# Kernel tuning notes

Measured on AMD Instinct MI355X. Metric: run time of the kernel, lower is better.

The kernel has to match this reference:

```python
import jax, jax.numpy as jnp
import numpy as np

DIM = 1024
NUM_HEADS = 16
HEAD_DIM = DIM // NUM_HEADS
SCALE = HEAD_DIM ** (-0.5)


def setup_inputs() -> dict:
    key = jax.random.key(0)
    ks = jax.random.split(key, 5)
    B, N, C = 2, 2048, DIM
    q = jax.random.normal(ks[0], (B, N, C), dtype=jnp.float32)
    k = jax.random.normal(ks[1], (B, N, C), dtype=jnp.float32)
    v = jax.random.normal(ks[2], (B, N, C), dtype=jnp.float32)
    # fused qkv Linear weight, torch layout [3*C, C]; no bias (qkv_bias=False)
    qkv_w = jax.random.normal(ks[3], (3 * C, C), dtype=jnp.float32) * (C ** -0.5)
    proj_w = jax.random.normal(ks[4], (C, C), dtype=jnp.float32) * (C ** -0.5)
    proj_b = jnp.zeros((C,), dtype=jnp.float32)
    return {"q": q, "k": k, "v": v, "qkv_w": qkv_w, "proj_w": proj_w,
            "proj_b": proj_b, "use_mask": 1}


def reference(q, k, v, qkv_w, proj_w, proj_b, use_mask):
    B, N, C = q.shape
    N_k = k.shape[1]
    H, hd = NUM_HEADS, HEAD_DIM
    # The original applies the full fused qkv Linear to each of q,k,v and keeps
    # only slice 0/1/2 respectively; computing just the used slice is identical math.
    wq, wk, wv = qkv_w[:C], qkv_w[C:2 * C], qkv_w[2 * C:]
    qh = (q @ wq.T).reshape(B, N, H, hd).transpose(0, 2, 1, 3)      # [B,H,N,hd]
    kh = (k @ wk.T).reshape(B, N_k, H, hd).transpose(0, 2, 1, 3)    # [B,H,Nk,hd]
    vh = (v @ wv.T).reshape(B, N_k, H, hd).transpose(0, 2, 1, 3)    # [B,H,Nk,hd]
    attn = jnp.einsum('bhnd,bhmd->bhnm', qh, kh) * SCALE            # [B,H,N,Nk]
    if use_mask:  # static Python flag -> causal tril mask as in the source
        msk = jnp.tril(jnp.ones((N, N_k), dtype=bool))
        attn = jnp.where(msk[None, None], attn, jnp.float32(-1e9))
    attn = jax.nn.softmax(attn, axis=-1)
    x = jnp.einsum('bhnm,bhmd->bhnd', attn, vh)                     # [B,H,N,hd]
    x = x.transpose(0, 2, 1, 3).reshape(B, N, C)
    x = x @ proj_w.T + proj_b
    return x, attn
```

## Files before the change

### kernel.cpp

```cpp
#include <hip/hip_runtime.h>


typedef unsigned short u16;
typedef unsigned int u32;
typedef __attribute__((ext_vector_type(8))) short s16x8;
typedef __attribute__((ext_vector_type(4))) float f32x4;
typedef __attribute__((ext_vector_type(4))) u16 u16x4;

#define AS1 __attribute__((address_space(1)))
#define AS3 __attribute__((address_space(3)))

static __device__ __forceinline__ u16 f2bf(float f) {
  u32 u = __builtin_bit_cast(u32, f);
  u = (u + 0x7fffu + ((u >> 16) & 1u)) >> 16;
  return (u16)u;
}

static __device__ __forceinline__ void gll16(const u16* g, u16* l) {
  __builtin_amdgcn_global_load_lds((const AS1 u32*)g, (AS3 u32*)l, 16, 0, 0);
}

static __device__ __forceinline__ f32x4 mfma_bf16(s16x8 a, s16x8 b, f32x4 c) {
  return __builtin_amdgcn_mfma_f32_16x16x32_bf16(a, b, c, 0, 0, 0);
}

__global__ __launch_bounds__(256) void cast_all_kernel(
    const float* __restrict__ q, const float* __restrict__ k, const float* __restrict__ v,
    const float* __restrict__ qkv_w, const float* __restrict__ proj_w,
    u16* __restrict__ qb, u16* __restrict__ kb, u16* __restrict__ vb,
    u16* __restrict__ wb, u16* __restrict__ pwb) {
  int i = blockIdx.x * 256 + threadIdx.x;
  const float* src; u16* dst; int off;
  if (i < 1048576)       { src = q;      dst = qb;  off = i; }
  else if (i < 2097152)  { src = k;      dst = kb;  off = i - 1048576; }
  else if (i < 3145728)  { src = v;      dst = vb;  off = i - 2097152; }
  else if (i < 3932160)  { src = qkv_w;  dst = wb;  off = i - 3145728; }
  else if (i < 4194304)  { src = proj_w; dst = pwb; off = i - 3932160; }
  else return;
  f32x4 vv = ((const f32x4*)src)[off];
  u16x4 o = { f2bf(vv.x), f2bf(vv.y), f2bf(vv.z), f2bf(vv.w) };
  ((u16x4*)dst)[off] = o;
}

static __device__ __forceinline__ void gemm_core_1024(
    const u16* __restrict__ A, const u16* __restrict__ Bm,
    int m0, int n0, int t, u16* a_s, u16* b_s, f32x4 acc[4][4]) {
  const int lane = t & 63;
  const int w = t >> 6;
  const int wm = (w & 1) * 64, wn = (w >> 1) * 64;
  const int lrow = lane & 15, lq = lane >> 4;
  const int r0 = t >> 2;
  const int c0 = (t & 3) * 8;

  for (int kt = 0; kt < 1024; kt += 32) {
    __syncthreads();
    gll16(A  + (size_t)(m0 + r0)      * 1024 + kt + c0, &a_s[(size_t)t * 8]);
    gll16(A  + (size_t)(m0 + r0 + 64) * 1024 + kt + c0, &a_s[(size_t)(t + 256) * 8]);
    gll16(Bm + (size_t)(n0 + r0)      * 1024 + kt + c0, &b_s[(size_t)t * 8]);
    gll16(Bm + (size_t)(n0 + r0 + 64) * 1024 + kt + c0, &b_s[(size_t)(t + 256) * 8]);
    __syncthreads();
    s16x8 af[4], bfr[4];
#pragma unroll
    for (int x = 0; x < 4; x++) af[x]  = *(const s16x8*)&a_s[(wm + x*16 + lrow)*32 + lq*8];
#pragma unroll
    for (int x = 0; x < 4; x++) bfr[x] = *(const s16x8*)&b_s[(wn + x*16 + lrow)*32 + lq*8];
#pragma unroll
    for (int tm = 0; tm < 4; tm++)
#pragma unroll
      for (int tn = 0; tn < 4; tn++)
        acc[tm][tn] = mfma_bf16(af[tm], bfr[tn], acc[tm][tn]);
  }
}

__global__ __launch_bounds__(256) void gemm_qkv_kernel(
    const u16* __restrict__ qb, const u16* __restrict__ kb, const u16* __restrict__ vb,
    const u16* __restrict__ wb, u16* __restrict__ Qh, u16* __restrict__ Kh,
    u16* __restrict__ Vt) {
  __shared__ u16 a_s[128*32], b_s[128*32];
  const int mode = blockIdx.z;
  const u16* A = (mode == 0) ? qb : (mode == 1) ? kb : vb;
  const u16* Bm = wb + (size_t)mode * (1024 * 1024);
  const int m0 = blockIdx.y * 128, n0 = blockIdx.x * 128;
  const int t = threadIdx.x;
  f32x4 acc[4][4];
  const f32x4 Z = {0.f, 0.f, 0.f, 0.f};
#pragma unroll
  for (int i = 0; i < 4; i++)
#pragma unroll
    for (int j = 0; j < 4; j++) acc[i][j] = Z;

  gemm_core_1024(A, Bm, m0, n0, t, a_s, b_s, acc);

  const int lane = t & 63, w = t >> 6;
  const int wm = (w & 1) * 64, wn = (w >> 1) * 64;
  const int lrow = lane & 15, lq = lane >> 4;
#pragma unroll
  for (int tm = 0; tm < 4; tm++) {
#pragma unroll
    for (int tn = 0; tn < 4; tn++) {
      const int ng = n0 + wn + tn * 16 + lrow;
      const int h = ng >> 6, d = ng & 63;
#pragma unroll
      for (int i = 0; i < 4; i++) {
        const int mg = m0 + wm + tm * 16 + lq * 4 + i;
        const int b = mg >> 11, s = mg & 2047;
        const float v = acc[tm][tn][i];
        if (mode == 0)
          Qh[((size_t)(b * 16 + h) * 2048 + s) * 64 + d] = f2bf(v * 0.125f);
        else if (mode == 1)
          Kh[((size_t)(b * 16 + h) * 2048 + s) * 64 + d] = f2bf(v);
        else
          Vt[((size_t)(b * 16 + h) * 64 + d) * 2048 + s] = f2bf(v);
      }
    }
  }
}

__global__ __launch_bounds__(256) void gemm_proj_kernel(
    const u16* __restrict__ xatt, const u16* __restrict__ pwb,
    const float* __restrict__ bias, float* __restrict__ out) {
  __shared__ u16 a_s[128*32], b_s[128*32];
  const int m0 = blockIdx.y * 128, n0 = blockIdx.x * 128;
  const int t = threadIdx.x;
  f32x4 acc[4][4];
  const f32x4 Z = {0.f, 0.f, 0.f, 0.f};
#pragma unroll
  for (int i = 0; i < 4; i++)
#pragma unroll
    for (int j = 0; j < 4; j++) acc[i][j] = Z;

  gemm_core_1024(xatt, pwb, m0, n0, t, a_s, b_s, acc);

  const int lane = t & 63, w = t >> 6;
  const int wm = (w & 1) * 64, wn = (w >> 1) * 64;
  const int lrow = lane & 15, lq = lane >> 4;
#pragma unroll
  for (int tn = 0; tn < 4; tn++) {
    const int ng = n0 + wn + tn * 16 + lrow;
    const float bv = bias[ng];
#pragma unroll
    for (int tm = 0; tm < 4; tm++) {
#pragma unroll
      for (int i = 0; i < 4; i++) {
        const int mg = m0 + wm + tm * 16 + lq * 4 + i;
        out[(size_t)mg * 1024 + ng] = acc[tm][tn][i] + bv;
      }
    }
  }
}


static __device__ __forceinline__ void qk_tile(const s16x8 qf[2], const s16x8 kf[4][2],
                                               f32x4 sacc[4]) {
  const f32x4 Z = {0.f, 0.f, 0.f, 0.f};
#pragma unroll
  for (int tn = 0; tn < 4; tn++) {
    sacc[tn] = Z;
#pragma unroll
    for (int kq = 0; kq < 2; kq++)
      sacc[tn] = mfma_bf16(qf[kq], kf[tn][kq], sacc[tn]);
  }
}

static __device__ __forceinline__ void expsum_tile(const f32x4 sacc[4], bool diag,
                                                   int lrow, int rbase, float l_acc[4]) {
  float part[4] = {0.f, 0.f, 0.f, 0.f};
#pragma unroll
  for (int tn = 0; tn < 4; tn++)
#pragma unroll
    for (int i = 0; i < 4; i++) {
      const bool ok = !diag || (tn * 16 + lrow <= rbase + i);
      part[i] += ok ? __expf(sacc[tn][i]) : 0.f;
    }
#pragma unroll
  for (int i = 0; i < 4; i++) {
    float s = part[i];
    s += __shfl_xor(s, 1, 16);
    s += __shfl_xor(s, 2, 16);
    s += __shfl_xor(s, 4, 16);
    s += __shfl_xor(s, 8, 16);
    l_acc[i] += s;
  }
}

static __device__ __forceinline__ void p_phase(const f32x4 sacc[4], bool diag,
                                               int lane, int lrow, int lq, int w,
                                               const float invl[4], float* pw,
                                               float* __restrict__ gb, s16x8 pf[2]) {
#pragma unroll
  for (int tn = 0; tn < 4; tn++)
#pragma unroll
    for (int i = 0; i < 4; i++) {
      const int rl = lq * 4 + i;
      const bool ok = !diag || (tn * 16 + lrow <= w * 16 + rl);
      const float pv = ok ? __expf(sacc[tn][i]) * invl[i] : 0.f;
      pw[rl * 68 + tn * 16 + lrow] = pv;
    }
  const int rr = lane >> 3, c8 = (lane & 7) * 4;
#pragma unroll
  for (int j = 0; j < 2; j++)
#pragma unroll
    for (int m = 0; m < 2; m++) {
      f32x4 vv = *(const f32x4*)&pw[(rr + 8 * j) * 68 + m * 32 + c8];
      *(f32x4*)&gb[(size_t)(rr + 8 * j) * 2048 + m * 32 + c8] = vv;
    }
#pragma unroll
  for (int kq = 0; kq < 2; kq++) {
    f32x4 lo = *(const f32x4*)&pw[lrow * 68 + kq * 32 + lq * 8];
    f32x4 hi = *(const f32x4*)&pw[lrow * 68 + kq * 32 + lq * 8 + 4];
    s16x8 r;
    r[0] = (short)f2bf(lo.x); r[1] = (short)f2bf(lo.y);
    r[2] = (short)f2bf(lo.z); r[3] = (short)f2bf(lo.w);
    r[4] = (short)f2bf(hi.x); r[5] = (short)f2bf(hi.y);
    r[6] = (short)f2bf(hi.z); r[7] = (short)f2bf(hi.w);
    pf[kq] = r;
  }
}

__global__ __launch_bounds__(256, 2) void attn_kernel(
    const u16* __restrict__ Qh, const u16* __restrict__ Kh, const u16* __restrict__ Vt,
    float* __restrict__ attn, u16* __restrict__ xatt, const int* __restrict__ use_mask_p) {
  __shared__ u16 smem[8192 + 8192];
  __shared__ float p32[4][16 * 68];
  u16* k_s = smem;
  u16* vq  = smem + 8192;

  const int bh = blockIdx.y;
  const int p  = blockIdx.x;
  const int t = threadIdx.x;
  const int lane = t & 63, w = t >> 6;
  const int lrow = lane & 15, lq = lane >> 4;
  const int use_mask = *use_mask_p;

  const int q0[2] = { p * 64, (31 - p) * 64 };
  const int Tc[2] = { use_mask ? p : 31, use_mask ? 31 - p : 31 };
  const int Tmax  = Tc[1];

  const int rs  = t >> 3;
  const int csw = (((t & 7) ^ (rs & 7)) * 8);
  const int sk  = (lrow & 7) << 3;

  const u16* kg = Kh + (size_t)bh * (2048 * 64);
  const u16* vg = Vt + (size_t)bh * (64 * 2048);

  {
    const u16* qgA = Qh + ((size_t)bh * 2048 + q0[0]) * 64;
    const u16* qgB = Qh + ((size_t)bh * 2048 + q0[1]) * 64;
    gll16(qgA + (size_t)rs * 64 + csw,        &vq[t * 8]);
    gll16(qgA + (size_t)(rs + 32) * 64 + csw, &vq[(t + 256) * 8]);
    gll16(qgB + (size_t)rs * 64 + csw,        &vq[4096 + t * 8]);
    gll16(qgB + (size_t)(rs + 32) * 64 + csw, &vq[4096 + (t + 256) * 8]);
    gll16(kg + (size_t)rs * 64 + csw,         &k_s[t * 8]);
    gll16(kg + (size_t)(rs + 32) * 64 + csw,  &k_s[(t + 256) * 8]);
  }
  __syncthreads();

  s16x8 qf[2][2];
  const int qrow = w * 16 + lrow;
#pragma unroll
  for (int kq = 0; kq < 2; kq++) {
    qf[0][kq] = *(const s16x8*)&vq[qrow * 64 + ((kq * 32 + lq * 8) ^ sk)];
    qf[1][kq] = *(const s16x8*)&vq[4096 + qrow * 64 + ((kq * 32 + lq * 8) ^ sk)];
  }

  const int rbase = w * 16 + lq * 4;

  float l_acc[2][4];
#pragma unroll
  for (int c = 0; c < 2; c++)
#pragma unroll
    for (int i = 0; i < 4; i++) l_acc[c][i] = 0.f;

  for (int tt = 0; tt <= Tmax; tt++) {
    const int cur = tt & 1;
    if (tt < Tmax) {
      gll16(kg + (size_t)((tt + 1) * 64 + rs) * 64 + csw,      &k_s[(cur ^ 1) * 4096 + t * 8]);
      gll16(kg + (size_t)((tt + 1) * 64 + rs + 32) * 64 + csw, &k_s[(cur ^ 1) * 4096 + (t + 256) * 8]);
    }
    s16x8 kf[4][2];
#pragma unroll
    for (int tn = 0; tn < 4; tn++)
#pragma unroll
      for (int kq = 0; kq < 2; kq++)
        kf[tn][kq] = *(const s16x8*)&k_s[cur * 4096 + (tn * 16 + lrow) * 64 + ((kq * 32 + lq * 8) ^ sk)];
    f32x4 sacc[4];
    __builtin_amdgcn_s_setprio(1);
    qk_tile(qf[1], kf, sacc);
    __builtin_amdgcn_s_setprio(0);
    expsum_tile(sacc, use_mask && (tt == Tc[1]), lrow, rbase, l_acc[1]);
    if (tt <= Tc[0]) {
      __builtin_amdgcn_s_setprio(1);
      qk_tile(qf[0], kf, sacc);
      __builtin_amdgcn_s_setprio(0);
      expsum_tile(sacc, use_mask && (tt == Tc[0]), lrow, rbase, l_acc[0]);
    }
    __syncthreads();
  }

  float inv_l[2][4];
#pragma unroll
  for (int c = 0; c < 2; c++)
#pragma unroll
    for (int i = 0; i < 4; i++) inv_l[c][i] = 1.0f / l_acc[c][i];

  f32x4 oacc[2][4];
  const f32x4 Z = {0.f, 0.f, 0.f, 0.f};
#pragma unroll
  for (int c = 0; c < 2; c++)
#pragma unroll
    for (int i = 0; i < 4; i++) oacc[c][i] = Z;

  gll16(kg + (size_t)rs * 64 + csw,          &k_s[t * 8]);
  gll16(kg + (size_t)(rs + 32) * 64 + csw,   &k_s[(t + 256) * 8]);
  gll16(vg + (size_t)rs * 2048 + csw,        &vq[t * 8]);
  gll16(vg + (size_t)(rs + 32) * 2048 + csw, &vq[(t + 256) * 8]);
  __syncthreads();

  float* pw = &p32[w][0];

  for (int tt = 0; tt <= Tmax; tt++) {
    const int cur = tt & 1;
    if (tt < Tmax) {
      gll16(kg + (size_t)((tt + 1) * 64 + rs) * 64 + csw,        &k_s[(cur ^ 1) * 4096 + t * 8]);
      gll16(kg + (size_t)((tt + 1) * 64 + rs + 32) * 64 + csw,   &k_s[(cur ^ 1) * 4096 + (t + 256) * 8]);
      gll16(vg + (size_t)rs * 2048 + (tt + 1) * 64 + csw,        &vq[(cur ^ 1) * 4096 + t * 8]);
      gll16(vg + (size_t)(rs + 32) * 2048 + (tt + 1) * 64 + csw, &vq[(cur ^ 1) * 4096 + (t + 256) * 8]);
    }
    const bool act0 = (tt <= Tc[0]);
    s16x8 kf[4][2];
#pragma unroll
    for (int tn = 0; tn < 4; tn++)
#pragma unroll
      for (int kq = 0; kq < 2; kq++)
        kf[tn][kq] = *(const s16x8*)&k_s[cur * 4096 + (tn * 16 + lrow) * 64 + ((kq * 32 + lq * 8) ^ sk)];
    s16x8 vf[4][2];
#pragma unroll
    for (int td = 0; td < 4; td++)
#pragma unroll
      for (int kq = 0; kq < 2; kq++)
        vf[td][kq] = *(const s16x8*)&vq[cur * 4096 + (td * 16 + lrow) * 64 + ((kq * 32 + lq * 8) ^ sk)];

    {
      f32x4 sacc[4];
      __builtin_amdgcn_s_setprio(1);
      qk_tile(qf[1], kf, sacc);
      __builtin_amdgcn_s_setprio(0);
      s16x8 pf[2];
      float* gb = attn + ((size_t)(bh * 2048 + q0[1] + w * 16)) * 2048 + tt * 64;
      p_phase(sacc, use_mask && (tt == Tc[1]), lane, lrow, lq, w, inv_l[1], pw, gb, pf);
      __builtin_amdgcn_s_setprio(1);
#pragma unroll
      for (int td = 0; td < 4; td++)
#pragma unroll
        for (int kq = 0; kq < 2; kq++)
          oacc[1][td] = mfma_bf16(pf[kq], vf[td][kq], oacc[1][td]);
      __builtin_amdgcn_s_setprio(0);
    }
    if (act0) {
      f32x4 sacc[4];
      __builtin_amdgcn_s_setprio(1);
      qk_tile(qf[0], kf, sacc);
      __builtin_amdgcn_s_setprio(0);
      s16x8 pf[2];
      float* gb = attn + ((size_t)(bh * 2048 + q0[0] + w * 16)) * 2048 + tt * 64;
      p_phase(sacc, use_mask && (tt == Tc[0]), lane, lrow, lq, w, inv_l[0], pw, gb, pf);
      __builtin_amdgcn_s_setprio(1);
#pragma unroll
      for (int td = 0; td < 4; td++)
#pragma unroll
        for (int kq = 0; kq < 2; kq++)
          oacc[0][td] = mfma_bf16(pf[kq], vf[td][kq], oacc[0][td]);
      __builtin_amdgcn_s_setprio(0);
    }
    __syncthreads();
  }

  const int b = bh >> 4, h = bh & 15;
#pragma unroll
  for (int c = 0; c < 2; c++)
#pragma unroll
    for (int td = 0; td < 4; td++)
#pragma unroll
      for (int i = 0; i < 4; i++) {
        const int row = q0[c] + w * 16 + lq * 4 + i;
        xatt[((size_t)(b * 2048 + row)) * 1024 + h * 64 + td * 16 + lrow] = f2bf(oacc[c][td][i]);
      }

  if (use_mask) {
    const f32x4 Z4 = {0.f, 0.f, 0.f, 0.f};
    const int rr = t >> 3;
    const int c8 = (t & 7) * 4;
#pragma unroll
    for (int c = 0; c < 2; c++) {
      const int zc0 = q0[c] + 64;
      if (zc0 < 2048) {
        const int n32 = (2048 - zc0) >> 5;
        float* zb = attn + ((size_t)bh * 2048 + q0[c]) * 2048 + zc0;
        for (int j = 0; j < n32; j++) {
          *(f32x4*)&zb[(size_t)rr * 2048 + j * 32 + c8] = Z4;
          *(f32x4*)&zb[(size_t)(rr + 32) * 2048 + j * 32 + c8] = Z4;
        }
      }
    }
  }
}

extern "C" void kernel_launch(void* const* d_in, const int* in_sizes, int n_in,
                              void* d_out, int out_size, void* d_ws, size_t ws_size,
                              hipStream_t stream) {
  const float* q      = (const float*)d_in[0];
  const float* k      = (const float*)d_in[1];
  const float* v      = (const float*)d_in[2];
  const float* qkv_w  = (const float*)d_in[3];
  const float* proj_w = (const float*)d_in[4];
  const float* proj_b = (const float*)d_in[5];
  const int*   use_mask = (const int*)d_in[6];

  const size_t MB = 1024 * 1024;
  char* ws = (char*)d_ws;
  u16* qb  = (u16*)(ws + 0 * MB);
  u16* kb  = (u16*)(ws + 8 * MB);
  u16* vb  = (u16*)(ws + 16 * MB);
  u16* wb  = (u16*)(ws + 24 * MB);
  u16* pwb = (u16*)(ws + 30 * MB);
  u16* Qh  = (u16*)(ws + 32 * MB);
  u16* Kh  = (u16*)(ws + 40 * MB);
  u16* Vt  = (u16*)(ws + 48 * MB);
  u16* xat = qb;

  float* out_x    = (float*)d_out;
  float* out_attn = out_x + (size_t)2 * 2048 * 1024;

  cast_all_kernel<<<16384, 256, 0, stream>>>(q, k, v, qkv_w, proj_w, qb, kb, vb, wb, pwb);

  gemm_qkv_kernel<<<dim3(8, 32, 3), 256, 0, stream>>>(qb, kb, vb, wb, Qh, Kh, Vt);
  attn_kernel<<<dim3(16, 32), 256, 0, stream>>>(Qh, Kh, Vt, out_attn, xat, use_mask);
  gemm_proj_kernel<<<dim3(8, 32), 256, 0, stream>>>(xat, pwb, proj_b, out_x);
}
```

Before: 715.2 us.

## Load attention K/V/Q fragments directly from global and vectorize Vt stores

```diff
diff --git a/kernel.cpp b/kernel.cpp
--- a/kernel.cpp
+++ b/kernel.cpp
@@ -100,17 +100,23 @@
     for (int tn = 0; tn < 4; tn++) {
       const int ng = n0 + wn + tn * 16 + lrow;
       const int h = ng >> 6, d = ng & 63;
-#pragma unroll
-      for (int i = 0; i < 4; i++) {
-        const int mg = m0 + wm + tm * 16 + lq * 4 + i;
+      if (mode == 2) {
+        const int mg = m0 + wm + tm * 16 + lq * 4;
         const int b = mg >> 11, s = mg & 2047;
-        const float v = acc[tm][tn][i];
-        if (mode == 0)
-          Qh[((size_t)(b * 16 + h) * 2048 + s) * 64 + d] = f2bf(v * 0.125f);
-        else if (mode == 1)
-          Kh[((size_t)(b * 16 + h) * 2048 + s) * 64 + d] = f2bf(v);
-        else
-          Vt[((size_t)(b * 16 + h) * 64 + d) * 2048 + s] = f2bf(v);
+        u16x4 o = { f2bf(acc[tm][tn][0]), f2bf(acc[tm][tn][1]),
+                    f2bf(acc[tm][tn][2]), f2bf(acc[tm][tn][3]) };
+        *(u16x4*)&Vt[((size_t)(b * 16 + h) * 64 + d) * 2048 + s] = o;
+      } else {
+#pragma unroll
+        for (int i = 0; i < 4; i++) {
+          const int mg = m0 + wm + tm * 16 + lq * 4 + i;
+          const int b = mg >> 11, s = mg & 2047;
+          const float v = acc[tm][tn][i];
+          if (mode == 0)
+            Qh[((size_t)(b * 16 + h) * 2048 + s) * 64 + d] = f2bf(v * 0.125f);
+          else
+            Kh[((size_t)(b * 16 + h) * 2048 + s) * 64 + d] = f2bf(v);
+        }
       }
     }
   }
@@ -220,10 +226,7 @@
 __global__ __launch_bounds__(256, 2) void attn_kernel(
     const u16* __restrict__ Qh, const u16* __restrict__ Kh, const u16* __restrict__ Vt,
     float* __restrict__ attn, u16* __restrict__ xatt, const int* __restrict__ use_mask_p) {
-  __shared__ u16 smem[8192 + 8192];
   __shared__ float p32[4][16 * 68];
-  u16* k_s = smem;
-  u16* vq  = smem + 8192;
 
   const int bh = blockIdx.y;
   const int p  = blockIdx.x;
@@ -236,32 +239,16 @@
   const int Tc[2] = { use_mask ? p : 31, use_mask ? 31 - p : 31 };
   const int Tmax  = Tc[1];
 
-  const int rs  = t >> 3;
-  const int csw = (((t & 7) ^ (rs & 7)) * 8);
-  const int sk  = (lrow & 7) << 3;
-
   const u16* kg = Kh + (size_t)bh * (2048 * 64);
   const u16* vg = Vt + (size_t)bh * (64 * 2048);
 
-  {
-    const u16* qgA = Qh + ((size_t)bh * 2048 + q0[0]) * 64;
-    const u16* qgB = Qh + ((size_t)bh * 2048 + q0[1]) * 64;
-    gll16(qgA + (size_t)rs * 64 + csw,        &vq[t * 8]);
-    gll16(qgA + (size_t)(rs + 32) * 64 + csw, &vq[(t + 256) * 8]);
-    gll16(qgB + (size_t)rs * 64 + csw,        &vq[4096 + t * 8]);
-    gll16(qgB + (size_t)(rs + 32) * 64 + csw, &vq[4096 + (t + 256) * 8]);
-    gll16(kg + (size_t)rs * 64 + csw,         &k_s[t * 8]);
-    gll16(kg + (size_t)(rs + 32) * 64 + csw,  &k_s[(t + 256) * 8]);
-  }
-  __syncthreads();
-
   s16x8 qf[2][2];
-  const int qrow = w * 16 + lrow;
-#pragma unroll
-  for (int kq = 0; kq < 2; kq++) {
-    qf[0][kq] = *(const s16x8*)&vq[qrow * 64 + ((kq * 32 + lq * 8) ^ sk)];
-    qf[1][kq] = *(const s16x8*)&vq[4096 + qrow * 64 + ((kq * 32 + lq * 8) ^ sk)];
-  }
+#pragma unroll
+  for (int c = 0; c < 2; c++)
+#pragma unroll
+    for (int kq = 0; kq < 2; kq++)
+      qf[c][kq] = *(const s16x8*)&Qh[((size_t)bh * 2048 + q0[c] + w * 16 + lrow) * 64
+                                     + kq * 32 + lq * 8];
 
   const int rbase = w * 16 + lq * 4;
 
@@ -272,17 +259,13 @@
     for (int i = 0; i < 4; i++) l_acc[c][i] = 0.f;
 
   for (int tt = 0; tt <= Tmax; tt++) {
-    const int cur = tt & 1;
-    if (tt < Tmax) {
-      gll16(kg + (size_t)((tt + 1) * 64 + rs) * 64 + csw,      &k_s[(cur ^ 1) * 4096 + t * 8]);
-      gll16(kg + (size_t)((tt + 1) * 64 + rs + 32) * 64 + csw, &k_s[(cur ^ 1) * 4096 + (t + 256) * 8]);
-    }
     s16x8 kf[4][2];
 #pragma unroll
     for (int tn = 0; tn < 4; tn++)
 #pragma unroll
       for (int kq = 0; kq < 2; kq++)
-        kf[tn][kq] = *(const s16x8*)&k_s[cur * 4096 + (tn * 16 + lrow) * 64 + ((kq * 32 + lq * 8) ^ sk)];
+        kf[tn][kq] = *(const s16x8*)&kg[(size_t)(tt * 64 + tn * 16 + lrow) * 64
+                                        + kq * 32 + lq * 8];
     f32x4 sacc[4];
     __builtin_amdgcn_s_setprio(1);
     qk_tile(qf[1], kf, sacc);
@@ -294,7 +277,6 @@
       __builtin_amdgcn_s_setprio(0);
       expsum_tile(sacc, use_mask && (tt == Tc[0]), lrow, rbase, l_acc[0]);
     }
-    __syncthreads();
   }
 
   float inv_l[2][4];
@@ -310,35 +292,25 @@
 #pragma unroll
     for (int i = 0; i < 4; i++) oacc[c][i] = Z;
 
-  gll16(kg + (size_t)rs * 64 + csw,          &k_s[t * 8]);
-  gll16(kg + (size_t)(rs + 32) * 64 + csw,   &k_s[(t + 256) * 8]);
-  gll16(vg + (size_t)rs * 2048 + csw,        &vq[t * 8]);
-  gll16(vg + (size_t)(rs + 32) * 2048 + csw, &vq[(t + 256) * 8]);
-  __syncthreads();
-
   float* pw = &p32[w][0];
 
   for (int tt = 0; tt <= Tmax; tt++) {
-    const int cur = tt & 1;
-    if (tt < Tmax) {
-      gll16(kg + (size_t)((tt + 1) * 64 + rs) * 64 + csw,        &k_s[(cur ^ 1) * 4096 + t * 8]);
-      gll16(kg + (size_t)((tt + 1) * 64 + rs + 32) * 64 + csw,   &k_s[(cur ^ 1) * 4096 + (t + 256) * 8]);
-      gll16(vg + (size_t)rs * 2048 + (tt + 1) * 64 + csw,        &vq[(cur ^ 1) * 4096 + t * 8]);
-      gll16(vg + (size_t)(rs + 32) * 2048 + (tt + 1) * 64 + csw, &vq[(cur ^ 1) * 4096 + (t + 256) * 8]);
-    }
+    s16x8 kf[4][2];
+#pragma unroll
+    for (int tn = 0; tn < 4; tn++)
+#pragma unroll
+      for (int kq = 0; kq < 2; kq++)
+        kf[tn][kq] = *(const s16x8*)&kg[(size_t)(tt * 64 + tn * 16 + lrow) * 64
+                                        + kq * 32 + lq * 8];
+    s16x8 vf[4][2];
+#pragma unroll
+    for (int td = 0; td < 4; td++)
+#pragma unroll
+      for (int kq = 0; kq < 2; kq++)
+        vf[td][kq] = *(const s16x8*)&vg[(size_t)(td * 16 + lrow) * 2048 + tt * 64
+                                        + kq * 32 + lq * 8];
+
     const bool act0 = (tt <= Tc[0]);
-    s16x8 kf[4][2];
-#pragma unroll
-    for (int tn = 0; tn < 4; tn++)
-#pragma unroll
-      for (int kq = 0; kq < 2; kq++)
-        kf[tn][kq] = *(const s16x8*)&k_s[cur * 4096 + (tn * 16 + lrow) * 64 + ((kq * 32 + lq * 8) ^ sk)];
-    s16x8 vf[4][2];
-#pragma unroll
-    for (int td = 0; td < 4; td++)
-#pragma unroll
-      for (int kq = 0; kq < 2; kq++)
-        vf[td][kq] = *(const s16x8*)&vq[cur * 4096 + (td * 16 + lrow) * 64 + ((kq * 32 + lq * 8) ^ sk)];
 
     {
       f32x4 sacc[4];
@@ -372,7 +344,6 @@
           oacc[0][td] = mfma_bf16(pf[kq], vf[td][kq], oacc[0][td]);
       __builtin_amdgcn_s_setprio(0);
     }
-    __syncthreads();
   }
 
   const int b = bh >> 4, h = bh & 15;
```

Measured after the change: 790.9 us. 1.11x slower.
